# Kernel optimization log

Hardware: AMD Instinct MI355X
Metric: run time of the kernel (lower is better)

Reference implementation:

```python
import jax, jax.numpy as jnp
import numpy as np

B, H, W, C = 32, 56, 56, 256
NH, WS, SH = 8, 7, 3
HD = C // NH
SCALE = HD ** -0.5
N = WS * WS
MLP = 4 * C


def _rel_pos_index():
    coords = np.stack(np.meshgrid(np.arange(WS), np.arange(WS), indexing='ij')).reshape(2, -1)
    rel = (coords[:, :, None] - coords[:, None, :]).transpose(1, 2, 0)
    rel[..., 0] += WS - 1
    rel[..., 1] += WS - 1
    rel[..., 0] *= 2 * WS - 1
    return jnp.asarray(rel.sum(-1))  # (N, N) int


def _attn_mask():
    # standard Swin shifted-window mask, computed statically
    img = np.zeros((H, W))
    cnt = 0
    for hs in (slice(0, -WS), slice(-WS, -SH), slice(-SH, None)):
        for ws_ in (slice(0, -WS), slice(-WS, -SH), slice(-SH, None)):
            img[hs, ws_] = cnt
            cnt += 1
    mw = img.reshape(H // WS, WS, W // WS, WS).transpose(0, 2, 1, 3).reshape(-1, N)
    am = mw[:, None, :] - mw[:, :, None]
    am = np.where(am != 0, -1e9, 0.0).astype(np.float32)
    return jnp.asarray(am)  # (nW, N, N)


def _part(x):
    b = x.shape[0]
    x = x.reshape(b, H // WS, WS, W // WS, WS, C)
    return x.transpose(0, 1, 3, 2, 4, 5).reshape(-1, N, C)


def _rev(xw):
    x = xw.reshape(-1, H // WS, W // WS, WS, WS, C)
    return x.transpose(0, 1, 3, 2, 4, 5).reshape(-1, H, W, C)


def _ln(x, g, b):
    m = x.mean(-1, keepdims=True)
    v = x.var(-1, keepdims=True)
    return (x - m) / jnp.sqrt(v + 1e-5) * g + b


def setup_inputs() -> dict:
    key = jax.random.key(0)
    ks = jax.random.split(key, 6)
    s = 0.02
    return {
        'x': jax.random.normal(ks[0], (B, H, W, C), jnp.float32),
        'gamma1': jnp.ones((C,), jnp.float32),
        'beta1': jnp.zeros((C,), jnp.float32),
        'w_qkv': jax.random.normal(ks[1], (C, 3 * C), jnp.float32) * s,
        'b_qkv': jnp.zeros((3 * C,), jnp.float32),
        'rpb': jax.random.normal(ks[2], ((2 * WS - 1) ** 2, NH), jnp.float32) * s,
        'w_proj': jax.random.normal(ks[3], (C, C), jnp.float32) * s,
        'b_proj': jnp.zeros((C,), jnp.float32),
        'gamma2': jnp.ones((C,), jnp.float32),
        'beta2': jnp.zeros((C,), jnp.float32),
        'w_fc1': jax.random.normal(ks[4], (C, MLP), jnp.float32) * s,
        'b_fc1': jnp.zeros((MLP,), jnp.float32),
        'w_fc2': jax.random.normal(ks[5], (MLP, C), jnp.float32) * s,
        'b_fc2': jnp.zeros((C,), jnp.float32),
    }


def reference(x, gamma1, beta1, w_qkv, b_qkv, rpb, w_proj, b_proj, gamma2, beta2, w_fc1, b_fc1, w_fc2, b_fc2):
    idx = _rel_pos_index()
    mask = _attn_mask()  # (nW, N, N)
    nW = mask.shape[0]

    shortcut = x
    xn = _ln(x, gamma1, beta1)
    xs = jnp.roll(xn, (-SH, -SH), axis=(1, 2))        # cyclic shift
    xw = _part(xs)                                     # (B*nW, N, C)

    qkv = (xw @ w_qkv + b_qkv).reshape(-1, N, 3, NH, HD).transpose(2, 0, 3, 1, 4)
    # SNN-variant IF (ReLU) gates on q, k, v
    q, k, v = jax.nn.relu(qkv[0]), jax.nn.relu(qkv[1]), jax.nn.relu(qkv[2])

    attn = jnp.einsum('bhnd,bhmd->bhnm', q * SCALE, k)  # (B*nW, NH, N, N)
    bias = rpb[idx].transpose(2, 0, 1)                  # (NH, N, N)
    attn = attn + bias[None]
    attn = attn.reshape(-1, nW, NH, N, N) + mask[None, :, None]
    attn = attn.reshape(-1, NH, N, N)
    # stdp_qk ReLU before softmax (faithful to source)
    attn = jax.nn.softmax(jax.nn.relu(attn), axis=-1)
    # stdp_av ReLU on attention output
    out = jax.nn.relu(jnp.einsum('bhnm,bhmd->bhnd', attn, v))
    out = out.transpose(0, 2, 1, 3).reshape(-1, N, C) @ w_proj + b_proj

    xs = _rev(out)
    x = shortcut + jnp.roll(xs, (SH, SH), axis=(1, 2))  # reverse shift + residual

    h = jax.nn.gelu(_ln(x, gamma2, beta2) @ w_fc1 + b_fc1, approximate=False)
    return x + h @ w_fc2 + b_fc2
```

## Files before the change

kernel.cpp:

```cpp
#include <hip/hip_runtime.h>
#include <stdint.h>

typedef unsigned short u16;
typedef short bf16x8 __attribute__((ext_vector_type(8)));
typedef float f32x4 __attribute__((ext_vector_type(4)));

#define NTOK 100352
#define NWIN 2048
#define CC 256
#define NHEAD 8
#define HDIM 32
#define NWT 49
#define MLPD 1024
#define ATT_SCALE 0.17677669529663687f

__device__ __forceinline__ u16 f2b(float f) {
  union { float f; uint32_t u; } c; c.f = f;
  return (u16)((c.u + 0x7fffu + ((c.u >> 16) & 1u)) >> 16);
}
__device__ __forceinline__ float b2f(u16 h) {
  union { uint32_t u; float f; } c; c.u = ((uint32_t)h) << 16;
  return c.f;
}
__device__ __forceinline__ uint32_t f2b2(float lo, float hi) {
  uint32_t r;
  asm("v_cvt_pk_bf16_f32 %0, %1, %2" : "=v"(r) : "v"(lo), "v"(hi));
  return r;
}

__device__ __forceinline__ void gload_lds16(const void* g, void* l) {
  __builtin_amdgcn_global_load_lds((const __attribute__((address_space(1))) void*)g,
                                   (__attribute__((address_space(3))) void*)l, 16, 0, 0);
}

__global__ __launch_bounds__(256)
void prep_k(const float* __restrict__ wqkv, const float* __restrict__ wproj,
            const float* __restrict__ wfc1, const float* __restrict__ wfc2,
            const float* __restrict__ rpb,
            u16* __restrict__ qkvT, u16* __restrict__ projT,
            u16* __restrict__ fc1T, u16* __restrict__ fc2T, float* __restrict__ lut) {
  int i = blockIdx.x * 256 + threadIdx.x;
  if (i < 196608) {
    int k = i / 768, n = i % 768;
    qkvT[(size_t)n * 256 + k] = f2b(wqkv[i]);
  } else if (i < 262144) {
    int j = i - 196608, k = j / 256, n = j % 256;
    projT[(size_t)n * 256 + k] = f2b(wproj[j]);
  } else if (i < 524288) {
    int j = i - 262144, k = j / 1024, n = j % 1024;
    fc1T[(size_t)n * 256 + k] = f2b(wfc1[j]);
  } else if (i < 786432) {
    int j = i - 524288, k = j / 256, n = j % 256;
    fc2T[(size_t)n * 1024 + k] = f2b(wfc2[j]);
  } else if (i < 819200) {
    int j = i - 786432;
    int h = j >> 12, m = (j >> 6) & 63, n = j & 63;
    float v = 0.f;
    if (m < 49 && n < 49) {
      int i1 = n / 7, j1 = n % 7, i2 = m / 7, j2 = m % 7;
      v = rpb[((i1 - i2 + 6) * 13 + (j1 - j2 + 6)) * 8 + h];
    }
    lut[j] = v;
  }
}

__global__ __launch_bounds__(256)
void ln_k(const float* __restrict__ x, const float* __restrict__ g,
          const float* __restrict__ be, u16* __restrict__ out) {
  int token = blockIdx.x * 4 + (threadIdx.x >> 6);
  int lane = threadIdx.x & 63;
  int win = token / 49, nn = token % 49;
  int b = win >> 6, wh = (win >> 3) & 7, ww = win & 7;
  int i = nn / 7, j = nn % 7;
  int h = wh * 7 + i + 3; if (h >= 56) h -= 56;
  int w = ww * 7 + j + 3; if (w >= 56) w -= 56;
  size_t src = ((size_t)((b * 56 + h) * 56 + w)) * CC;
  f32x4 v = *(const f32x4*)&x[src + lane * 4];
  float s1 = v[0] + v[1] + v[2] + v[3];
  float s2 = v[0]*v[0] + v[1]*v[1] + v[2]*v[2] + v[3]*v[3];
#pragma unroll
  for (int o = 32; o; o >>= 1) { s1 += __shfl_xor(s1, o); s2 += __shfl_xor(s2, o); }
  float mean = s1 * (1.f / 256.f);
  float var = s2 * (1.f / 256.f) - mean * mean;
  float rstd = rsqrtf(var + 1e-5f);
  f32x4 gv = *(const f32x4*)&g[lane * 4];
  f32x4 bv = *(const f32x4*)&be[lane * 4];
  float y0 = (v[0]-mean)*rstd*gv[0] + bv[0];
  float y1 = (v[1]-mean)*rstd*gv[1] + bv[1];
  float y2 = (v[2]-mean)*rstd*gv[2] + bv[2];
  float y3 = (v[3]-mean)*rstd*gv[3] + bv[3];
  *(uint2*)&out[(size_t)token * CC + lane * 4] = make_uint2(f2b2(y0, y1), f2b2(y2, y3));
}

#define BM 128
#define BN 128
enum { EPI_QKV = 0, EPI_GELU = 2, EPI_FC2 = 3 };

template<int EPI, int NKT>
__global__ __launch_bounds__(256)
void gemm_k(const u16* __restrict__ A, const u16* __restrict__ BT,
            const float* __restrict__ bias,
            void* __restrict__ p0, const void* __restrict__ p1, int row0) {
  constexpr int K = NKT * 64;
  __shared__ u16 aL[2][BM * 64];
  __shared__ u16 bL[BN * 64];
  const int tid = threadIdx.x;
  const int lane = tid & 63;
  const int wv = tid >> 6;
  const int wm = wv >> 1, wn = wv & 1;

  int bx = blockIdx.x, by = blockIdx.y;
  {
    int nwg = gridDim.x * gridDim.y;
    int lin = by * gridDim.x + bx;
    int q = nwg >> 3, r = nwg & 7;
    int xcd = lin & 7, idx = lin >> 3;
    int wg = (xcd < r ? xcd * (q + 1) : r * (q + 1) + (xcd - r) * q) + idx;
    bx = wg % gridDim.x;
    by = wg / gridDim.x;
  }
  const long m0 = (long)by * BM;
  const int n0 = bx * BN;

  f32x4 acc[4][4] = {};
  const int r15 = lane & 15;
  const int g4 = lane >> 4;

  const u16* pA[4];
  const u16* pB[4];
  int lslot[4];
#pragma unroll
  for (int it = 0; it < 4; ++it) {
    int slot = tid + 256 * it;
    int row = slot >> 3, c8 = slot & 7;
    int cs = c8 ^ (row & 7);
    pA[it] = &A[(m0 + row) * K + cs * 8];
    pB[it] = &BT[(size_t)(n0 + row) * K + cs * 8];
    lslot[it] = slot * 8;
  }
  int aoff[2][4], boff[2][4];
#pragma unroll
  for (int kk = 0; kk < 2; ++kk)
#pragma unroll
    for (int m = 0; m < 4; ++m) {
      int rowa = wm * 64 + m * 16 + r15;
      aoff[kk][m] = rowa * 64 + (((kk * 4 + g4) ^ (rowa & 7)) << 3);
      int rowb = wn * 64 + m * 16 + r15;
      boff[kk][m] = rowb * 64 + (((kk * 4 + g4) ^ (rowb & 7)) << 3);
    }

  auto stageA = [&](int bufi) {
#pragma unroll
    for (int it = 0; it < 4; ++it) { gload_lds16(pA[it], &aL[bufi][lslot[it]]); pA[it] += 64; }
  };
  auto stageB = [&]() {
#pragma unroll
    for (int it = 0; it < 4; ++it) { gload_lds16(pB[it], &bL[lslot[it]]); pB[it] += 64; }
  };

  stageB();
  stageA(0);
  stageA(1);

  for (int t = 0; t < NKT; ++t) {
    if (t + 1 < NKT) asm volatile("s_waitcnt vmcnt(4)" ::: "memory");
    else             asm volatile("s_waitcnt vmcnt(0)" ::: "memory");
    __builtin_amdgcn_sched_barrier(0);
    __builtin_amdgcn_s_barrier();
    __builtin_amdgcn_sched_barrier(0);
    {
      const u16* ab = aL[t & 1];
#pragma unroll
      for (int kk = 0; kk < 2; ++kk) {
        bf16x8 af[4], bfr[4];
#pragma unroll
        for (int m = 0; m < 4; ++m) af[m] = *(const bf16x8*)&ab[aoff[kk][m]];
#pragma unroll
        for (int n = 0; n < 4; ++n) bfr[n] = *(const bf16x8*)&bL[boff[kk][n]];
#pragma unroll
        for (int n = 0; n < 4; ++n)
#pragma unroll
          for (int m = 0; m < 4; ++m)
            acc[n][m] = __builtin_amdgcn_mfma_f32_16x16x32_bf16(bfr[n], af[m], acc[n][m], 0, 0, 0);
      }
    }
    __builtin_amdgcn_sched_barrier(0);
    __builtin_amdgcn_s_barrier();
    __builtin_amdgcn_sched_barrier(0);
    if (t + 1 < NKT) stageB();
    if (t + 2 < NKT) stageA(t & 1);
  }

#pragma unroll
  for (int mt = 0; mt < 4; ++mt) {
    const int mrow = (int)m0 + wm * 64 + mt * 16 + r15;
    int win = 0, nn = 0;
    size_t pix = 0;
    if (EPI == EPI_QKV) { win = mrow / 49; nn = mrow - win * 49; }
    if (EPI == EPI_FC2) {
      int token = row0 + mrow;
      win = token / 49; nn = token - win * 49;
      int b = win >> 6, wh = (win >> 3) & 7, ww = win & 7;
      int i = nn / 7, jj = nn - i * 7;
      int h = wh * 7 + i + 3; if (h >= 56) h -= 56;
      int w = ww * 7 + jj + 3; if (w >= 56) w -= 56;
      pix = (size_t)((b * 56 + h) * 56 + w);
    }
#pragma unroll
    for (int nt = 0; nt < 4; ++nt) {
      const int col0 = n0 + wn * 64 + nt * 16 + g4 * 4;
      f32x4 bv = *(const f32x4*)&bias[col0];
      f32x4 v;
#pragma unroll
      for (int j = 0; j < 4; ++j) v[j] = acc[nt][mt][j] + bv[j];
      if (EPI == EPI_QKV) {
        int s = col0 >> 8, head = (col0 >> 5) & 7, d0 = col0 & 31;
        float sc = (s == 0) ? ATT_SCALE : 1.f;
#pragma unroll
        for (int j = 0; j < 4; ++j) v[j] = fmaxf(v[j], 0.f) * sc;
        u16* dst = (u16*)p0 + (size_t)s * ((size_t)NTOK * CC);
        *(uint2*)&dst[(((size_t)(win * NHEAD + head)) * NWT + nn) * HDIM + d0] =
            make_uint2(f2b2(v[0], v[1]), f2b2(v[2], v[3]));
      } else if (EPI == EPI_GELU) {
#pragma unroll
        for (int j = 0; j < 4; ++j) {
          float u = 0.79788456f * (v[j] + 0.044715f * v[j] * v[j] * v[j]);
          float th = 1.f - 2.f / (__expf(2.f * u) + 1.f);
          v[j] = 0.5f * v[j] * (1.f + th);
        }
        *(uint2*)&((u16*)p0)[(size_t)mrow * MLPD + col0] =
            make_uint2(f2b2(v[0], v[1]), f2b2(v[2], v[3]));
      } else {
        uint2 rb = *(const uint2*)&((const u16*)p1)[(size_t)(row0 + mrow) * CC + col0];
        v[0] += b2f((u16)(rb.x & 0xffffu));
        v[1] += b2f((u16)(rb.x >> 16));
        v[2] += b2f((u16)(rb.y & 0xffffu));
        v[3] += b2f((u16)(rb.y >> 16));
        *(f32x4*)&((float*)p0)[pix * CC + col0] = v;
      }
    }
  }
}

__global__ __launch_bounds__(512)
void gemm_ln_k(const u16* __restrict__ A, const u16* __restrict__ BT,
               const float* __restrict__ bias, const float* __restrict__ xres,
               const float* __restrict__ g2, const float* __restrict__ be2,
               u16* __restrict__ x2, u16* __restrict__ xn2) {
  constexpr int K = 256;
  constexpr int NKT = 4;
  __shared__ u16 aL[2][128 * 64];
  __shared__ u16 bL[256 * 64];
  __shared__ float st[4 * 128 * 2];
  const int tid = threadIdx.x;
  const int lane = tid & 63;
  const int wv = tid >> 6;
  const int wm = wv >> 2;
  const int wn = wv & 3;
  const int r15 = lane & 15;
  const int g4 = lane >> 4;

  int by = blockIdx.x;
  {
    int nwg = gridDim.x;
    int q = nwg >> 3, r = nwg & 7;
    int xcd = by & 7, idx = by >> 3;
    by = (xcd < r ? xcd * (q + 1) : r * (q + 1) + (xcd - r) * q) + idx;
  }
  const long m0 = (long)by * 128;

  f32x4 acc[4][4] = {};

  const u16* pA[2];
  int la[2];
#pragma unroll
  for (int it = 0; it < 2; ++it) {
    int slot = tid + 512 * it;
    int row = slot >> 3, c8 = slot & 7;
    int cs = c8 ^ (row & 7);
    pA[it] = &A[(m0 + row) * K + cs * 8];
    la[it] = slot * 8;
  }
  const u16* pB[4];
  int lb[4];
#pragma unroll
  for (int it = 0; it < 4; ++it) {
    int slot = tid + 512 * it;
    int row = slot >> 3, c8 = slot & 7;
    int cs = c8 ^ (row & 7);
    pB[it] = &BT[(size_t)row * K + cs * 8];
    lb[it] = slot * 8;
  }
  int aoff[2][4], boff[2][4];
#pragma unroll
  for (int kk = 0; kk < 2; ++kk)
#pragma unroll
    for (int m = 0; m < 4; ++m) {
      int rowa = wm * 64 + m * 16 + r15;
      aoff[kk][m] = rowa * 64 + (((kk * 4 + g4) ^ (rowa & 7)) << 3);
      int rowb = wn * 64 + m * 16 + r15;
      boff[kk][m] = rowb * 64 + (((kk * 4 + g4) ^ (rowb & 7)) << 3);
    }

  auto stageA = [&](int bufi) {
#pragma unroll
    for (int it = 0; it < 2; ++it) { gload_lds16(pA[it], &aL[bufi][la[it]]); pA[it] += 64; }
  };
  auto stageB = [&]() {
#pragma unroll
    for (int it = 0; it < 4; ++it) { gload_lds16(pB[it], &bL[lb[it]]); pB[it] += 64; }
  };

  stageB();
  stageA(0);
  stageA(1);

  for (int t = 0; t < NKT; ++t) {
    if (t + 1 < NKT) asm volatile("s_waitcnt vmcnt(2)" ::: "memory");
    else             asm volatile("s_waitcnt vmcnt(0)" ::: "memory");
    __builtin_amdgcn_sched_barrier(0);
    __builtin_amdgcn_s_barrier();
    __builtin_amdgcn_sched_barrier(0);
    {
      const u16* ab = aL[t & 1];
#pragma unroll
      for (int kk = 0; kk < 2; ++kk) {
        bf16x8 af[4], bfr[4];
#pragma unroll
        for (int m = 0; m < 4; ++m) af[m] = *(const bf16x8*)&ab[aoff[kk][m]];
#pragma unroll
        for (int n = 0; n < 4; ++n) bfr[n] = *(const bf16x8*)&bL[boff[kk][n]];
#pragma unroll
        for (int n = 0; n < 4; ++n)
#pragma unroll
          for (int m = 0; m < 4; ++m)
            acc[n][m] = __builtin_amdgcn_mfma_f32_16x16x32_bf16(bfr[n], af[m], acc[n][m], 0, 0, 0);
      }
    }
    __builtin_amdgcn_sched_barrier(0);
    __builtin_amdgcn_s_barrier();
    __builtin_amdgcn_sched_barrier(0);
    if (t + 1 < NKT) stageB();
    if (t + 2 < NKT) stageA(t & 1);
  }

  size_t pix[4];
  float s1[4] = {}, s2[4] = {};
#pragma unroll
  for (int mt = 0; mt < 4; ++mt) {
    const int mrow = (int)m0 + wm * 64 + mt * 16 + r15;
    int win = mrow / 49, nn = mrow - win * 49;
    int b = win >> 6, wh = (win >> 3) & 7, ww = win & 7;
    int i = nn / 7, jj = nn - i * 7;
    int h = wh * 7 + i + 3; if (h >= 56) h -= 56;
    int w = ww * 7 + jj + 3; if (w >= 56) w -= 56;
    pix[mt] = (size_t)((b * 56 + h) * 56 + w);
#pragma unroll
    for (int nt = 0; nt < 4; ++nt) {
      const int col0 = wn * 64 + nt * 16 + g4 * 4;
      f32x4 bv = *(const f32x4*)&bias[col0];
      f32x4 r = *(const f32x4*)&xres[pix[mt] * CC + col0];
      f32x4 v;
#pragma unroll
      for (int j = 0; j < 4; ++j) {
        v[j] = acc[nt][mt][j] + bv[j] + r[j];
        s1[mt] += v[j];
        s2[mt] += v[j] * v[j];
      }
      *(uint2*)&x2[(size_t)mrow * CC + col0] =
          make_uint2(f2b2(v[0], v[1]), f2b2(v[2], v[3]));
      acc[nt][mt] = v;
    }
    s1[mt] += __shfl_xor(s1[mt], 16);  s1[mt] += __shfl_xor(s1[mt], 32);
    s2[mt] += __shfl_xor(s2[mt], 16);  s2[mt] += __shfl_xor(s2[mt], 32);
    if (g4 == 0) {
      int wrow = wm * 64 + mt * 16 + r15;
      st[(wn * 128 + wrow) * 2 + 0] = s1[mt];
      st[(wn * 128 + wrow) * 2 + 1] = s2[mt];
    }
  }
  __syncthreads();
#pragma unroll
  for (int mt = 0; mt < 4; ++mt) {
    const int mrow = (int)m0 + wm * 64 + mt * 16 + r15;
    int wrow = wm * 64 + mt * 16 + r15;
    float t1 = 0.f, t2 = 0.f;
#pragma unroll
    for (int w2 = 0; w2 < 4; ++w2) {
      t1 += st[(w2 * 128 + wrow) * 2 + 0];
      t2 += st[(w2 * 128 + wrow) * 2 + 1];
    }
    float mean = t1 * (1.f / 256.f);
    float var = t2 * (1.f / 256.f) - mean * mean;
    float rstd = rsqrtf(var + 1e-5f);
#pragma unroll
    for (int nt = 0; nt < 4; ++nt) {
      const int col0 = wn * 64 + nt * 16 + g4 * 4;
      f32x4 gv = *(const f32x4*)&g2[col0];
      f32x4 bv = *(const f32x4*)&be2[col0];
      float y0 = (acc[nt][mt][0] - mean) * rstd * gv[0] + bv[0];
      float y1 = (acc[nt][mt][1] - mean) * rstd * gv[1] + bv[1];
      float y2 = (acc[nt][mt][2] - mean) * rstd * gv[2] + bv[2];
      float y3 = (acc[nt][mt][3] - mean) * rstd * gv[3] + bv[3];
      *(uint2*)&xn2[(size_t)mrow * CC + col0] = make_uint2(f2b2(y0, y1), f2b2(y2, y3));
    }
  }
}

__global__ __launch_bounds__(256)
void attn_mfma_k(const u16* __restrict__ q, const u16* __restrict__ k2,
                 const u16* __restrict__ v2, const float* __restrict__ lut,
                 u16* __restrict__ out) {
  __shared__ u16 P_lds[4][64 * 72];
  const int tid = threadIdx.x;
  const int wv = tid >> 6;
  const int lane = tid & 63;
  const int c = lane & 15;
  const int g = lane >> 4;
  const int blk = blockIdx.x * 4 + wv;
  const int head = blk & 7;
  const int win = blk >> 3;
  const int wimg = win & 63;
  const int wh = wimg >> 3, ww = wimg & 7;
  const size_t base = (size_t)blk * (NWT * HDIM);
  u16* Pw = P_lds[wv];

  bf16x8 kf[4], qf[4];
#pragma unroll
  for (int t = 0; t < 4; ++t) {
    kf[t] = *(const bf16x8*)&k2[base + (size_t)(t * 16 + c) * HDIM + g * 8];
    qf[t] = *(const bf16x8*)&q [base + (size_t)(t * 16 + c) * HDIM + g * 8];
  }
  bf16x8 vf[2][2];
#pragma unroll
  for (int kcc = 0; kcc < 2; ++kcc)
#pragma unroll
    for (int td = 0; td < 2; ++td)
#pragma unroll
      for (int jj = 0; jj < 8; ++jj) {
        int m = kcc * 32 + g * 8 + jj;
        m = m < 49 ? m : 48;
        vf[kcc][td][jj] = (short)v2[base + (size_t)m * HDIM + td * 16 + c];
      }

  f32x4 acc[4][4] = {};
#pragma unroll
  for (int tm = 0; tm < 4; ++tm)
#pragma unroll
    for (int tn = 0; tn < 4; ++tn)
      acc[tm][tn] = __builtin_amdgcn_mfma_f32_16x16x32_bf16(kf[tm], qf[tn], acc[tm][tn], 0, 0, 0);

  const float* lrow = &lut[(size_t)head * 64 * 64];
  int Ln[4];
#pragma unroll
  for (int tn = 0; tn < 4; ++tn) {
    int n = tn * 16 + c;
    int i1 = (n * 9363) >> 16;
    int j1 = n - i1 * 7;
    int rh = (wh < 7) ? 0 : (i1 < 4 ? 1 : 2);
    int rw = (ww < 7) ? 0 : (j1 < 4 ? 1 : 2);
    Ln[tn] = rh * 3 + rw;
  }
  float colmax[4] = {0.f, 0.f, 0.f, 0.f};
#pragma unroll
  for (int tm = 0; tm < 4; ++tm)
#pragma unroll
    for (int j = 0; j < 4; ++j) {
      int m = tm * 16 + g * 4 + j;
      int i2 = (m * 9363) >> 16;
      int j2 = m - i2 * 7;
      int rh = (wh < 7) ? 0 : (i2 < 4 ? 1 : 2);
      int rw = (ww < 7) ? 0 : (j2 < 4 ? 1 : 2);
      int Lm = rh * 3 + rw;
#pragma unroll
      for (int tn = 0; tn < 4; ++tn) {
        float s = acc[tm][tn][j] + lrow[m * 64 + tn * 16 + c];
        s = fmaxf(s, 0.f);
        if (Lm != Ln[tn]) s = 0.f;
        acc[tm][tn][j] = s;
        colmax[tn] = fmaxf(colmax[tn], s);
      }
    }
#pragma unroll
  for (int tn = 0; tn < 4; ++tn) {
    colmax[tn] = fmaxf(colmax[tn], __shfl_xor(colmax[tn], 16));
    colmax[tn] = fmaxf(colmax[tn], __shfl_xor(colmax[tn], 32));
  }
  float colsum[4] = {0.f, 0.f, 0.f, 0.f};
#pragma unroll
  for (int tm = 0; tm < 4; ++tm)
#pragma unroll
    for (int j = 0; j < 4; ++j) {
      int m = tm * 16 + g * 4 + j;
      bool mvalid = (m < NWT);
#pragma unroll
      for (int tn = 0; tn < 4; ++tn) {
        float e = mvalid ? __expf(acc[tm][tn][j] - colmax[tn]) : 0.f;
        acc[tm][tn][j] = e;
        colsum[tn] += e;
      }
    }
#pragma unroll
  for (int tn = 0; tn < 4; ++tn) {
    colsum[tn] += __shfl_xor(colsum[tn], 16);
    colsum[tn] += __shfl_xor(colsum[tn], 32);
    colsum[tn] = 1.f / colsum[tn];
  }

#pragma unroll
  for (int tn = 0; tn < 4; ++tn) {
    int n = tn * 16 + c;
#pragma unroll
    for (int tm = 0; tm < 4; ++tm) {
      float r = colsum[tn];
      *(uint2*)&Pw[n * 72 + tm * 16 + g * 4] =
          make_uint2(f2b2(acc[tm][tn][0] * r, acc[tm][tn][1] * r),
                     f2b2(acc[tm][tn][2] * r, acc[tm][tn][3] * r));
    }
  }

  f32x4 oacc[4][2] = {};
#pragma unroll
  for (int kcc = 0; kcc < 2; ++kcc) {
    bf16x8 pf[4];
#pragma unroll
    for (int tr = 0; tr < 4; ++tr)
      pf[tr] = *(const bf16x8*)&Pw[(tr * 16 + c) * 72 + kcc * 32 + g * 8];
#pragma unroll
    for (int tr = 0; tr < 4; ++tr)
#pragma unroll
      for (int td = 0; td < 2; ++td)
        oacc[tr][td] = __builtin_amdgcn_mfma_f32_16x16x32_bf16(pf[tr], vf[kcc][td], oacc[tr][td], 0, 0, 0);
  }

#pragma unroll
  for (int tr = 0; tr < 4; ++tr)
#pragma unroll
    for (int j = 0; j < 4; ++j) {
      int n = tr * 16 + g * 4 + j;
      if (n < NWT) {
#pragma unroll
        for (int td = 0; td < 2; ++td) {
          int d = td * 16 + c;
          out[((size_t)(win * NWT + n)) * CC + head * HDIM + d] =
              f2b(fmaxf(oacc[tr][td][j], 0.f));
        }
      }
    }
}

extern "C" void kernel_launch(void* const* d_in, const int* in_sizes, int n_in,
                              void* d_out, int out_size, void* d_ws, size_t ws_size,
                              hipStream_t stream) {
  const float* x      = (const float*)d_in[0];
  const float* gamma1 = (const float*)d_in[1];
  const float* beta1  = (const float*)d_in[2];
  const float* w_qkv  = (const float*)d_in[3];
  const float* b_qkv  = (const float*)d_in[4];
  const float* rpb    = (const float*)d_in[5];
  const float* w_proj = (const float*)d_in[6];
  const float* b_proj = (const float*)d_in[7];
  const float* gamma2 = (const float*)d_in[8];
  const float* beta2  = (const float*)d_in[9];
  const float* w_fc1  = (const float*)d_in[10];
  const float* b_fc1  = (const float*)d_in[11];
  const float* w_fc2  = (const float*)d_in[12];
  const float* b_fc2  = (const float*)d_in[13];
  float* out = (float*)d_out;

  char* ws = (char*)d_ws;
  size_t off = 0;
  auto alloc = [&](size_t bytes) { void* p = ws + off; off = (off + bytes + 255) & ~(size_t)255; return p; };

  u16* wqkvT = (u16*)alloc(768 * 256 * 2);
  u16* wprojT = (u16*)alloc(256 * 256 * 2);
  u16* wfc1T = (u16*)alloc(1024 * 256 * 2);
  u16* wfc2T = (u16*)alloc(256 * 1024 * 2);
  float* lut = (float*)alloc(8 * 64 * 64 * 4);
  u16* region2 = (u16*)alloc((size_t)NTOK * CC * 2);
  char* region1 = (char*)alloc((size_t)3 * NTOK * CC * 2);

  u16* xw = region2;
  u16* qb = (u16*)region1;
  u16* kb = qb + (size_t)NTOK * CC;
  u16* vb = kb + (size_t)NTOK * CC;
  u16* attn_out = region2;
  u16* x2 = (u16*)region1;
  u16* xn2 = x2 + (size_t)NTOK * CC;
  u16* hbuf = region2;

  if (ws_size < off) return;

  prep_k<<<3200, 256, 0, stream>>>(w_qkv, w_proj, w_fc1, w_fc2, rpb,
                                   wqkvT, wprojT, wfc1T, wfc2T, lut);

  ln_k<<<NTOK / 4, 256, 0, stream>>>(x, gamma1, beta1, xw);

  gemm_k<EPI_QKV, 4><<<dim3(768 / BN, NTOK / BM), 256, 0, stream>>>(
      xw, wqkvT, b_qkv, (void*)qb, nullptr, 0);

  attn_mfma_k<<<NWIN * NHEAD / 4, 256, 0, stream>>>(qb, kb, vb, lut, attn_out);

  gemm_ln_k<<<NTOK / 128, 512, 0, stream>>>(
      attn_out, wprojT, b_proj, x, gamma2, beta2, x2, xn2);

  const int MCH = 25088;
  for (int c = 0; c < 4; ++c) {
    const u16* a1 = xn2 + (size_t)c * MCH * CC;
    gemm_k<EPI_GELU, 4><<<dim3(MLPD / BN, MCH / BM), 256, 0, stream>>>(
        a1, wfc1T, b_fc1, (void*)hbuf, nullptr, 0);
    gemm_k<EPI_FC2, 16><<<dim3(CC / BN, MCH / BM), 256, 0, stream>>>(
        hbuf, wfc2T, b_fc2, (void*)out, (const void*)x2, c * MCH);
  }
}
```

Before: 516.3 us.

## Fuse MLP fc1, GELU and fc2 into one kernel keeping hidden tile in LDS

```diff
diff --git a/kernel.cpp b/kernel.cpp
--- a/kernel.cpp
+++ b/kernel.cpp
@@ -94,13 +94,13 @@
 
 #define BM 128
 #define BN 128
-enum { EPI_QKV = 0, EPI_GELU = 2, EPI_FC2 = 3 };
+enum { EPI_QKV = 0 };
 
 template<int EPI, int NKT>
 __global__ __launch_bounds__(256)
 void gemm_k(const u16* __restrict__ A, const u16* __restrict__ BT,
             const float* __restrict__ bias,
-            void* __restrict__ p0, const void* __restrict__ p1, int row0) {
+            void* __restrict__ p0, const void* __restrict__ p1) {
   constexpr int K = NKT * 64;
   __shared__ u16 aL[2][BM * 64];
   __shared__ u16 bL[BN * 64];
@@ -194,18 +194,7 @@
 #pragma unroll
   for (int mt = 0; mt < 4; ++mt) {
     const int mrow = (int)m0 + wm * 64 + mt * 16 + r15;
-    int win = 0, nn = 0;
-    size_t pix = 0;
-    if (EPI == EPI_QKV) { win = mrow / 49; nn = mrow - win * 49; }
-    if (EPI == EPI_FC2) {
-      int token = row0 + mrow;
-      win = token / 49; nn = token - win * 49;
-      int b = win >> 6, wh = (win >> 3) & 7, ww = win & 7;
-      int i = nn / 7, jj = nn - i * 7;
-      int h = wh * 7 + i + 3; if (h >= 56) h -= 56;
-      int w = ww * 7 + jj + 3; if (w >= 56) w -= 56;
-      pix = (size_t)((b * 56 + h) * 56 + w);
-    }
+    int win = mrow / 49, nn = mrow - win * 49;
 #pragma unroll
     for (int nt = 0; nt < 4; ++nt) {
       const int col0 = n0 + wn * 64 + nt * 16 + g4 * 4;
@@ -213,31 +202,13 @@
       f32x4 v;
 #pragma unroll
       for (int j = 0; j < 4; ++j) v[j] = acc[nt][mt][j] + bv[j];
-      if (EPI == EPI_QKV) {
-        int s = col0 >> 8, head = (col0 >> 5) & 7, d0 = col0 & 31;
-        float sc = (s == 0) ? ATT_SCALE : 1.f;
-#pragma unroll
-        for (int j = 0; j < 4; ++j) v[j] = fmaxf(v[j], 0.f) * sc;
-        u16* dst = (u16*)p0 + (size_t)s * ((size_t)NTOK * CC);
-        *(uint2*)&dst[(((size_t)(win * NHEAD + head)) * NWT + nn) * HDIM + d0] =
-            make_uint2(f2b2(v[0], v[1]), f2b2(v[2], v[3]));
-      } else if (EPI == EPI_GELU) {
-#pragma unroll
-        for (int j = 0; j < 4; ++j) {
-          float u = 0.79788456f * (v[j] + 0.044715f * v[j] * v[j] * v[j]);
-          float th = 1.f - 2.f / (__expf(2.f * u) + 1.f);
-          v[j] = 0.5f * v[j] * (1.f + th);
-        }
-        *(uint2*)&((u16*)p0)[(size_t)mrow * MLPD + col0] =
-            make_uint2(f2b2(v[0], v[1]), f2b2(v[2], v[3]));
-      } else {
-        uint2 rb = *(const uint2*)&((const u16*)p1)[(size_t)(row0 + mrow) * CC + col0];
-        v[0] += b2f((u16)(rb.x & 0xffffu));
-        v[1] += b2f((u16)(rb.x >> 16));
-        v[2] += b2f((u16)(rb.y & 0xffffu));
-        v[3] += b2f((u16)(rb.y >> 16));
-        *(f32x4*)&((float*)p0)[pix * CC + col0] = v;
-      }
+      int s = col0 >> 8, head = (col0 >> 5) & 7, d0 = col0 & 31;
+      float sc = (s == 0) ? ATT_SCALE : 1.f;
+#pragma unroll
+      for (int j = 0; j < 4; ++j) v[j] = fmaxf(v[j], 0.f) * sc;
+      u16* dst = (u16*)p0 + (size_t)s * ((size_t)NTOK * CC);
+      *(uint2*)&dst[(((size_t)(win * NHEAD + head)) * NWT + nn) * HDIM + d0] =
+          make_uint2(f2b2(v[0], v[1]), f2b2(v[2], v[3]));
     }
   }
 }
@@ -403,6 +374,213 @@
       float y2 = (acc[nt][mt][2] - mean) * rstd * gv[2] + bv[2];
       float y3 = (acc[nt][mt][3] - mean) * rstd * gv[3] + bv[3];
       *(uint2*)&xn2[(size_t)mrow * CC + col0] = make_uint2(f2b2(y0, y1), f2b2(y2, y3));
+    }
+  }
+}
+
+__global__ __launch_bounds__(512, 4)
+void mlp_fused_k(const u16* __restrict__ xn, const u16* __restrict__ fc1T,
+                 const u16* __restrict__ fc2T, const float* __restrict__ b1,
+                 const float* __restrict__ b2v, const u16* __restrict__ x2,
+                 float* __restrict__ outp) {
+  __shared__ u16 lds[24576];
+  u16* shA0 = lds;
+  u16* shA1 = lds + 4096;
+  u16* shB1 = lds + 8192;
+  u16* shB2 = lds;
+  u16* shH  = lds + 16384;
+
+  const int tid = threadIdx.x;
+  const int lane = tid & 63;
+  const int wv = tid >> 6;
+  const int wmw = wv >> 2;
+  const int wnw = wv & 3;
+  const int r15 = lane & 15;
+  const int g4 = lane >> 4;
+
+  int by = blockIdx.x;
+  {
+    int nwg = gridDim.x;
+    int q = nwg >> 3, r = nwg & 7;
+    int xcd = by & 7, idx = by >> 3;
+    by = (xcd < r ? xcd * (q + 1) : r * (q + 1) + (xcd - r) * q) + idx;
+  }
+  const long m0 = (long)by * 64;
+
+  const int rowA = tid >> 3, csA = (tid & 7) ^ (rowA & 7);
+  const u16* pAbase = &xn[(m0 + rowA) * 256 + csA * 8];
+  int rowB1[2], lb1[2];
+  const u16* pB1base[2];
+#pragma unroll
+  for (int it = 0; it < 2; ++it) {
+    int slot = tid + 512 * it;
+    rowB1[it] = slot >> 3;
+    int cs = (slot & 7) ^ (rowB1[it] & 7);
+    pB1base[it] = &fc1T[(size_t)rowB1[it] * 256 + cs * 8];
+    lb1[it] = slot * 8;
+  }
+  int lb2[4];
+  const u16* pB2base[4];
+#pragma unroll
+  for (int it = 0; it < 4; ++it) {
+    int slot = tid + 512 * it;
+    int row = slot >> 3;
+    int cs = (slot & 7) ^ (row & 7);
+    pB2base[it] = &fc2T[(size_t)row * 1024 + cs * 8];
+    lb2[it] = slot * 8;
+  }
+
+  int a1off[2][2], b1off[2][2];
+#pragma unroll
+  for (int kk = 0; kk < 2; ++kk)
+#pragma unroll
+    for (int m = 0; m < 2; ++m) {
+      int ra = wmw * 32 + m * 16 + r15;
+      a1off[kk][m] = ra * 64 + (((kk * 4 + g4) ^ (ra & 7)) << 3);
+      int rb = wnw * 32 + m * 16 + r15;
+      b1off[kk][m] = rb * 64 + (((kk * 4 + g4) ^ (rb & 7)) << 3);
+    }
+  int b2off[2][4];
+#pragma unroll
+  for (int kk = 0; kk < 2; ++kk)
+#pragma unroll
+    for (int n = 0; n < 4; ++n) {
+      int rb = wnw * 64 + n * 16 + r15;
+      b2off[kk][n] = rb * 64 + (((kk * 4 + g4) ^ (rb & 7)) << 3);
+    }
+
+  f32x4 oacc[4][2] = {};
+
+  for (int hc = 0; hc < 8; ++hc) {
+    const size_t b1chunk = (size_t)hc * 128 * 256;
+    gload_lds16(pB1base[0] + b1chunk, &shB1[lb1[0]]);
+    gload_lds16(pB1base[1] + b1chunk, &shB1[lb1[1]]);
+    gload_lds16(pAbase,      &shA0[tid * 8]);
+    gload_lds16(pAbase + 64, &shA1[tid * 8]);
+
+    f32x4 acc1[2][2] = {};
+    for (int t = 0; t < 4; ++t) {
+      if (t + 1 < 4) asm volatile("s_waitcnt vmcnt(1)" ::: "memory");
+      else           asm volatile("s_waitcnt vmcnt(0)" ::: "memory");
+      __builtin_amdgcn_sched_barrier(0);
+      __builtin_amdgcn_s_barrier();
+      __builtin_amdgcn_sched_barrier(0);
+      {
+        const u16* ab = (t & 1) ? shA1 : shA0;
+#pragma unroll
+        for (int kk = 0; kk < 2; ++kk) {
+          bf16x8 af[2], bfr[2];
+#pragma unroll
+          for (int m = 0; m < 2; ++m) af[m] = *(const bf16x8*)&ab[a1off[kk][m]];
+#pragma unroll
+          for (int n = 0; n < 2; ++n) bfr[n] = *(const bf16x8*)&shB1[b1off[kk][n]];
+#pragma unroll
+          for (int n = 0; n < 2; ++n)
+#pragma unroll
+            for (int m = 0; m < 2; ++m)
+              acc1[n][m] = __builtin_amdgcn_mfma_f32_16x16x32_bf16(bfr[n], af[m], acc1[n][m], 0, 0, 0);
+        }
+      }
+      __builtin_amdgcn_sched_barrier(0);
+      __builtin_amdgcn_s_barrier();
+      __builtin_amdgcn_sched_barrier(0);
+      if (t + 1 < 4) {
+        gload_lds16(pB1base[0] + b1chunk + (t + 1) * 64, &shB1[lb1[0]]);
+        gload_lds16(pB1base[1] + b1chunk + (t + 1) * 64, &shB1[lb1[1]]);
+      }
+      if (t + 2 < 4) {
+        u16* dst = (t & 1) ? shA1 : shA0;
+        gload_lds16(pAbase + (t + 2) * 64, &dst[tid * 8]);
+      }
+    }
+    gload_lds16(pB2base[0] + hc * 128, &shB2[lb2[0]]);
+    gload_lds16(pB2base[1] + hc * 128, &shB2[lb2[1]]);
+    gload_lds16(pB2base[2] + hc * 128, &shB2[lb2[2]]);
+    gload_lds16(pB2base[3] + hc * 128, &shB2[lb2[3]]);
+
+#pragma unroll
+    for (int mt = 0; mt < 2; ++mt) {
+      const int hrow = wmw * 32 + mt * 16 + r15;
+#pragma unroll
+      for (int nt = 0; nt < 2; ++nt) {
+        const int col0 = wnw * 32 + nt * 16 + g4 * 4;
+        f32x4 bv = *(const f32x4*)&b1[hc * 128 + col0];
+        f32x4 v;
+#pragma unroll
+        for (int j = 0; j < 4; ++j) {
+          float u = acc1[nt][mt][j] + bv[j];
+          float t2 = 0.79788456f * (u + 0.044715f * u * u * u);
+          float th = 1.f - 2.f / (__expf(2.f * t2) + 1.f);
+          v[j] = 0.5f * u * (1.f + th);
+        }
+        int hidx = hrow * 128 + (((col0 >> 3) ^ (hrow & 15)) << 3) + (col0 & 4);
+        *(uint2*)&shH[hidx] = make_uint2(f2b2(v[0], v[1]), f2b2(v[2], v[3]));
+      }
+    }
+    asm volatile("s_waitcnt lgkmcnt(0)" ::: "memory");
+    __builtin_amdgcn_sched_barrier(0);
+    asm volatile("s_waitcnt vmcnt(0)" ::: "memory");
+    __builtin_amdgcn_sched_barrier(0);
+    __builtin_amdgcn_s_barrier();
+    __builtin_amdgcn_sched_barrier(0);
+
+#pragma unroll
+    for (int kt = 0; kt < 2; ++kt) {
+#pragma unroll
+      for (int kk = 0; kk < 2; ++kk) {
+        bf16x8 af[2], bfr[4];
+#pragma unroll
+        for (int m = 0; m < 2; ++m) {
+          int hrow = wmw * 32 + m * 16 + r15;
+          int kchunk = kt * 8 + kk * 4 + g4;
+          af[m] = *(const bf16x8*)&shH[hrow * 128 + ((kchunk ^ (hrow & 15)) << 3)];
+        }
+#pragma unroll
+        for (int n = 0; n < 4; ++n) bfr[n] = *(const bf16x8*)&shB2[b2off[kk][n]];
+#pragma unroll
+        for (int n = 0; n < 4; ++n)
+#pragma unroll
+          for (int m = 0; m < 2; ++m)
+            oacc[n][m] = __builtin_amdgcn_mfma_f32_16x16x32_bf16(bfr[n], af[m], oacc[n][m], 0, 0, 0);
+      }
+      __builtin_amdgcn_sched_barrier(0);
+      __builtin_amdgcn_s_barrier();
+      __builtin_amdgcn_sched_barrier(0);
+      if (kt == 0) {
+        gload_lds16(pB2base[0] + hc * 128 + 64, &shB2[lb2[0]]);
+        gload_lds16(pB2base[1] + hc * 128 + 64, &shB2[lb2[1]]);
+        gload_lds16(pB2base[2] + hc * 128 + 64, &shB2[lb2[2]]);
+        gload_lds16(pB2base[3] + hc * 128 + 64, &shB2[lb2[3]]);
+        asm volatile("s_waitcnt vmcnt(0)" ::: "memory");
+        __builtin_amdgcn_sched_barrier(0);
+        __builtin_amdgcn_s_barrier();
+        __builtin_amdgcn_sched_barrier(0);
+      }
+    }
+  }
+
+#pragma unroll
+  for (int mt = 0; mt < 2; ++mt) {
+    const int mrow = (int)m0 + wmw * 32 + mt * 16 + r15;
+    int win = mrow / 49, nn = mrow - win * 49;
+    int b = win >> 6, wh = (win >> 3) & 7, ww = win & 7;
+    int i = nn / 7, jj = nn - i * 7;
+    int h = wh * 7 + i + 3; if (h >= 56) h -= 56;
+    int w = ww * 7 + jj + 3; if (w >= 56) w -= 56;
+    size_t pix = (size_t)((b * 56 + h) * 56 + w);
+#pragma unroll
+    for (int nt = 0; nt < 4; ++nt) {
+      const int col0 = wnw * 64 + nt * 16 + g4 * 4;
+      f32x4 bv = *(const f32x4*)&b2v[col0];
+      f32x4 v;
+#pragma unroll
+      for (int j = 0; j < 4; ++j) v[j] = oacc[nt][mt][j] + bv[j];
+      uint2 rb = *(const uint2*)&x2[(size_t)mrow * CC + col0];
+      v[0] += b2f((u16)(rb.x & 0xffffu));
+      v[1] += b2f((u16)(rb.x >> 16));
+      v[2] += b2f((u16)(rb.y & 0xffffu));
+      v[3] += b2f((u16)(rb.y >> 16));
+      *(f32x4*)&outp[pix * CC + col0] = v;
     }
   }
 }
@@ -587,7 +765,6 @@
   u16* attn_out = region2;
   u16* x2 = (u16*)region1;
   u16* xn2 = x2 + (size_t)NTOK * CC;
-  u16* hbuf = region2;
 
   if (ws_size < off) return;
 
@@ -597,19 +774,13 @@
   ln_k<<<NTOK / 4, 256, 0, stream>>>(x, gamma1, beta1, xw);
 
   gemm_k<EPI_QKV, 4><<<dim3(768 / BN, NTOK / BM), 256, 0, stream>>>(
-      xw, wqkvT, b_qkv, (void*)qb, nullptr, 0);
+      xw, wqkvT, b_qkv, (void*)qb, nullptr);
 
   attn_mfma_k<<<NWIN * NHEAD / 4, 256, 0, stream>>>(qb, kb, vb, lut, attn_out);
 
   gemm_ln_k<<<NTOK / 128, 512, 0, stream>>>(
       attn_out, wprojT, b_proj, x, gamma2, beta2, x2, xn2);
 
-  const int MCH = 25088;
-  for (int c = 0; c < 4; ++c) {
-    const u16* a1 = xn2 + (size_t)c * MCH * CC;
-    gemm_k<EPI_GELU, 4><<<dim3(MLPD / BN, MCH / BM), 256, 0, stream>>>(
-        a1, wfc1T, b_fc1, (void*)hbuf, nullptr, 0);
-    gemm_k<EPI_FC2, 16><<<dim3(CC / BN, MCH / BM), 256, 0, stream>>>(
-        hbuf, wfc2T, b_fc2, (void*)out, (const void*)x2, c * MCH);
-  }
-}
+  mlp_fused_k<<<NTOK / 64, 512, 0, stream>>>(
+      xn2, wfc1T, wfc2T, b_fc1, b_fc2, x2, out);
+}
```

Measured after the change: 480.1 us. 7.0% less time.
